# Kernel tuning notes

Measured on AMD Instinct MI355X. Metric: run time of the kernel, lower is better.

Reference implementation:

```python
import jax, jax.numpy as jnp
import numpy as np

D = 384      # embedding_dim (module-level global)
H = 6        # num_heads
HD = D // H  # head_size = 64
T = 256      # block_size (tril buffer cap)
B = 128


def _layernorm(x, gamma, beta, eps=1e-5):
    mu = jnp.mean(x, axis=-1, keepdims=True)
    var = jnp.var(x, axis=-1, keepdims=True)
    return (x - mu) * jax.lax.rsqrt(var + eps) * gamma + beta


def setup_inputs() -> dict:
    key = jax.random.key(0)
    ks = jax.random.split(key, 12)
    s = 0.02
    return {
        "x":   jax.random.normal(ks[0], (B, T, D), jnp.float32),
        "Wq":  jax.random.normal(ks[1], (H, D, HD), jnp.float32) * s,
        "Wk":  jax.random.normal(ks[2], (H, D, HD), jnp.float32) * s,
        "Wv":  jax.random.normal(ks[3], (H, D, HD), jnp.float32) * s,
        "Wp":  jax.random.normal(ks[4], (D, D), jnp.float32) * s,
        "bp":  jnp.zeros((D,), jnp.float32),
        "W1":  jax.random.normal(ks[5], (D, 4 * D), jnp.float32) * s,
        "b1":  jnp.zeros((4 * D,), jnp.float32),
        "W2":  jax.random.normal(ks[6], (4 * D, D), jnp.float32) * s,
        "b2":  jnp.zeros((D,), jnp.float32),
        "g1":  jnp.ones((D,), jnp.float32),
        "be1": jnp.zeros((D,), jnp.float32),
        "g2":  jnp.ones((D,), jnp.float32),
        "be2": jnp.zeros((D,), jnp.float32),
    }


def reference(x, Wq, Wk, Wv, Wp, bp, W1, b1, W2, b2, g1, be1, g2, be2):
    Bsz, Tlen, C = x.shape
    # pre-LN self-attention
    h = _layernorm(x, g1, be1)
    q = jnp.einsum("btd,hdk->bhtk", h, Wq)
    k = jnp.einsum("bsd,hdk->bhsk", h, Wk)
    v = jnp.einsum("bsd,hdk->bhsk", h, Wv)
    # NOTE: source divides by sqrt(C)=sqrt(embedding_dim), not sqrt(head_size)
    scores = jnp.einsum("bhtk,bhsk->bhts", q, k) / jnp.sqrt(jnp.float32(C))
    causal = jnp.tril(jnp.ones((Tlen, Tlen), bool))
    scores = jnp.where(causal, scores, jnp.float32(-jnp.inf))
    attn = jax.nn.softmax(scores, axis=-1)          # dropout = identity (eval)
    o = jnp.einsum("bhts,bhsk->bhtk", attn, v)      # [B,H,T,HD]
    o = o.transpose(0, 2, 1, 3).reshape(Bsz, Tlen, C)  # concat heads
    sa = o @ Wp + bp
    x = x + sa
    # pre-LN feed-forward
    h2 = _layernorm(x, g2, be2)
    ff = jax.nn.relu(h2 @ W1 + b1) @ W2 + b2
    return x + ff
```

## Files before the change

### kernel.cpp

```cpp
#include <hip/hip_runtime.h>
#include <cstdint>
#include <cstddef>

#define D_   384
#define Hn   6
#define HDm  64
#define T_   256
#define B_   128
#define NROW (B_ * T_)

typedef __bf16  bf16x8 __attribute__((ext_vector_type(8)));
typedef float   f32x4  __attribute__((ext_vector_type(4)));
typedef const __attribute__((address_space(1))) void gvoid;
typedef __attribute__((address_space(3))) void lvoid;

__device__ inline uint32_t bf16rn(float f) {
  uint32_t u = __float_as_uint(f);
  return (u + 0x7FFFu + ((u >> 16) & 1u)) >> 16;
}

__global__ __launch_bounds__(128) void ln_kernel(const float* __restrict__ x,
                                                 const float* __restrict__ g,
                                                 const float* __restrict__ b,
                                                 uint16_t* __restrict__ out) {
  int row = blockIdx.x, tid = threadIdx.x;
  const float* xr = x + (size_t)row * D_;
  float v0 = xr[tid], v1 = xr[tid + 128], v2 = xr[tid + 256];
  float s  = v0 + v1 + v2;
  float ss = v0 * v0 + v1 * v1 + v2 * v2;
#pragma unroll
  for (int off = 32; off > 0; off >>= 1) {
    s  += __shfl_down(s, off);
    ss += __shfl_down(ss, off);
  }
  __shared__ float red[4];
  if ((tid & 63) == 0) { red[(tid >> 6) * 2] = s; red[(tid >> 6) * 2 + 1] = ss; }
  __syncthreads();
  float S = red[0] + red[2], SS = red[1] + red[3];
  float mu  = S * (1.0f / D_);
  float var = SS * (1.0f / D_) - mu * mu;
  float inv = rsqrtf(var + 1e-5f);
  uint16_t* orow = out + (size_t)row * D_;
  orow[tid]       = (uint16_t)bf16rn((v0 - mu) * inv * g[tid]       + b[tid]);
  orow[tid + 128] = (uint16_t)bf16rn((v1 - mu) * inv * g[tid + 128] + b[tid + 128]);
  orow[tid + 256] = (uint16_t)bf16rn((v2 - mu) * inv * g[tid + 256] + b[tid + 256]);
}

__global__ __launch_bounds__(256) void pack_qkv_w(const float* __restrict__ Wq,
                                                  const float* __restrict__ Wk,
                                                  const float* __restrict__ Wv,
                                                  uint16_t* __restrict__ Wo) {
  int idx = blockIdx.x * 256 + threadIdx.x;
  if (idx >= 1152 * D_) return;
  int col = idx / D_, d = idx % D_;
  int which = col / 384, c2 = col % 384;
  int h = c2 / HDm, k = c2 % HDm;
  const float* W = (which == 0) ? Wq : (which == 1) ? Wk : Wv;
  Wo[idx] = (uint16_t)bf16rn(W[((size_t)h * D_ + d) * HDm + k]);
}

__global__ __launch_bounds__(256) void pack_wt(const float* __restrict__ W,
                                               uint16_t* __restrict__ Wt,
                                               int K, int N) {
  int idx = blockIdx.x * 256 + threadIdx.x;
  if (idx >= K * N) return;
  int n = idx / K, k = idx % K;
  Wt[idx] = (uint16_t)bf16rn(W[(size_t)k * N + n]);
}

__global__ __launch_bounds__(256) void gemm_bf16(const uint16_t* __restrict__ A,
                                                 const uint16_t* __restrict__ Bt,
                                                 const float* __restrict__ bias,
                                                 const float* __restrict__ resid,
                                                 void* __restrict__ Cout,
                                                 int M, int N, int K,
                                                 int relu, int store_f32) {
  __shared__ uint16_t As[128 * 32];
  __shared__ uint16_t Bs[128 * 32];
  int tid = threadIdx.x;
  int bm = blockIdx.y * 128, bn = blockIdx.x * 128;
  int lane = tid & 63, wave = tid >> 6;
  int wm = (wave >> 1) << 6;
  int wn = (wave & 1) << 6;
  int lr = lane & 15;
  int lk = (lane >> 4) << 3;
  int r0 = (lane >> 4) << 2;

  f32x4 acc[4][4];
  const f32x4 zero = {0.f, 0.f, 0.f, 0.f};
#pragma unroll
  for (int i = 0; i < 4; ++i)
#pragma unroll
    for (int j = 0; j < 4; ++j) acc[i][j] = zero;

  for (int k0 = 0; k0 < K; k0 += 32) {
    __syncthreads();
#pragma unroll
    for (int t = 0; t < 2; ++t) {
      int c = t * 256 + tid;
      int row = c >> 2, kc = (c & 3) << 3;
      const uint16_t* ga = A  + (size_t)(bm + row) * K + (k0 + kc);
      const uint16_t* gb = Bt + (size_t)(bn + row) * K + (k0 + kc);
      __builtin_amdgcn_global_load_lds((gvoid*)ga, (lvoid*)((char*)As + c * 16), 16, 0, 0);
      __builtin_amdgcn_global_load_lds((gvoid*)gb, (lvoid*)((char*)Bs + c * 16), 16, 0, 0);
    }
    __syncthreads();

    bf16x8 af[4], bfr[4];
#pragma unroll
    for (int i = 0; i < 4; ++i)
      af[i] = *(const bf16x8*)&As[(wm + i * 16 + lr) * 32 + lk];
#pragma unroll
    for (int j = 0; j < 4; ++j)
      bfr[j] = *(const bf16x8*)&Bs[(wn + j * 16 + lr) * 32 + lk];
#pragma unroll
    for (int i = 0; i < 4; ++i)
#pragma unroll
      for (int j = 0; j < 4; ++j)
        acc[i][j] = __builtin_amdgcn_mfma_f32_16x16x32_bf16(af[i], bfr[j], acc[i][j], 0, 0, 0);
  }

#pragma unroll
  for (int i = 0; i < 4; ++i) {
#pragma unroll
    for (int r = 0; r < 4; ++r) {
      int rr = bm + wm + i * 16 + r0 + r;
#pragma unroll
      for (int j = 0; j < 4; ++j) {
        int col = bn + wn + j * 16 + lr;
        float v = acc[i][j][r];
        if (bias)  v += bias[col];
        if (relu)  v = fmaxf(v, 0.0f);
        if (resid) v += resid[(size_t)rr * N + col];
        if (store_f32) ((float*)Cout)[(size_t)rr * N + col] = v;
        else           ((uint16_t*)Cout)[(size_t)rr * N + col] = (uint16_t)bf16rn(v);
      }
    }
  }
}

__global__ __launch_bounds__(256, 2) void attn_mfma(const uint16_t* __restrict__ qkv,
                                                    uint16_t* __restrict__ o) {
  __shared__ uint16_t Kt[64 * 72];
  __shared__ uint16_t Vt[64 * 72];
  __shared__ uint16_t Pb[4 * 64 * 72];
  int bh = blockIdx.x;
  int b = bh / Hn, h = bh % Hn;
  int tid = threadIdx.x;
  int lane = tid & 63, w = tid >> 6;
  int ln = lane & 15, q = lane >> 4;
  int kq = q * 8;
  int m0 = w * 64;
  const uint16_t* base = qkv + (size_t)b * T_ * 1152;

  bf16x8 af[4][2];
#pragma unroll
  for (int i = 0; i < 4; ++i)
#pragma unroll
    for (int ks = 0; ks < 2; ++ks)
      af[i][ks] = *(const bf16x8*)(base + (size_t)(m0 + i * 16 + ln) * 1152 + h * HDm + ks * 32 + kq);

  f32x4 o_[4][4], m_[4], l_[4];
  const f32x4 zero = {0.f, 0.f, 0.f, 0.f};
#pragma unroll
  for (int i = 0; i < 4; ++i) {
    m_[i] = {-1e30f, -1e30f, -1e30f, -1e30f};
    l_[i] = zero;
#pragma unroll
    for (int n = 0; n < 4; ++n) o_[i][n] = zero;
  }
  const float cs = 0.07362222f;

  for (int jt = 0; jt < 4; ++jt) {
    if (jt) __syncthreads();
#pragma unroll
    for (int t = 0; t < 2; ++t) {
      int c = t * 256 + tid;
      int s = c >> 3, d0 = (c & 7) << 3;
      *(uint4*)&Kt[s * 72 + d0] =
          *(const uint4*)(base + (size_t)(jt * 64 + s) * 1152 + 384 + h * HDm + d0);
    }
    {
      int sv = tid & 63, dv = (tid >> 6) << 4;
      const uint16_t* gv = base + (size_t)(jt * 64 + sv) * 1152 + 768 + h * HDm + dv;
      uint16_t tmp[16];
      *(uint4*)&tmp[0] = *(const uint4*)gv;
      *(uint4*)&tmp[8] = *(const uint4*)(gv + 8);
#pragma unroll
      for (int jj = 0; jj < 16; ++jj) Vt[(dv + jj) * 72 + sv] = tmp[jj];
    }
    __syncthreads();

    if (w >= jt) {
      f32x4 s2[4][4];
#pragma unroll
      for (int i = 0; i < 4; ++i)
#pragma unroll
        for (int j = 0; j < 4; ++j) s2[i][j] = zero;
#pragma unroll
      for (int ks = 0; ks < 2; ++ks) {
        bf16x8 bf[4];
#pragma unroll
        for (int j = 0; j < 4; ++j)
          bf[j] = *(const bf16x8*)&Kt[(j * 16 + ln) * 72 + ks * 32 + kq];
#pragma unroll
        for (int i = 0; i < 4; ++i)
#pragma unroll
          for (int j = 0; j < 4; ++j)
            s2[i][j] = __builtin_amdgcn_mfma_f32_16x16x32_bf16(af[i][ks], bf[j], s2[i][j], 0, 0, 0);
      }
#pragma unroll
      for (int i = 0; i < 4; ++i) {
#pragma unroll
        for (int j = 0; j < 4; ++j)
#pragma unroll
          for (int r = 0; r < 4; ++r) s2[i][j][r] *= cs;
        if (jt == w) {
#pragma unroll
          for (int j = 0; j < 4; ++j)
#pragma unroll
            for (int r = 0; r < 4; ++r)
              if (j * 16 + ln > i * 16 + q * 4 + r) s2[i][j][r] = -1e30f;
        }
        f32x4 rm;
#pragma unroll
        for (int r = 0; r < 4; ++r)
          rm[r] = fmaxf(fmaxf(s2[i][0][r], s2[i][1][r]), fmaxf(s2[i][2][r], s2[i][3][r]));
#pragma unroll
        for (int off = 1; off < 16; off <<= 1)
#pragma unroll
          for (int r = 0; r < 4; ++r)
            rm[r] = fmaxf(rm[r], __shfl_xor(rm[r], off));
        f32x4 mn, al, ps;
#pragma unroll
        for (int r = 0; r < 4; ++r) {
          mn[r] = fmaxf(m_[i][r], rm[r]);
          al[r] = exp2f(m_[i][r] - mn[r]);
          ps[r] = 0.f;
        }
        m_[i] = mn;
#pragma unroll
        for (int j = 0; j < 4; ++j)
#pragma unroll
          for (int r = 0; r < 4; ++r) {
            float p = exp2f(s2[i][j][r] - mn[r]);
            s2[i][j][r] = p;
            ps[r] += p;
          }
#pragma unroll
        for (int r = 0; r < 4; ++r) l_[i][r] = l_[i][r] * al[r] + ps[r];
#pragma unroll
        for (int n = 0; n < 4; ++n)
#pragma unroll
          for (int r = 0; r < 4; ++r) o_[i][n][r] *= al[r];
#pragma unroll
        for (int j = 0; j < 4; ++j)
#pragma unroll
          for (int r = 0; r < 4; ++r)
            Pb[w * 4608 + (i * 16 + q * 4 + r) * 72 + j * 16 + ln] =
                (uint16_t)bf16rn(s2[i][j][r]);
      }
      bf16x8 pa[4][2];
#pragma unroll
      for (int i = 0; i < 4; ++i)
#pragma unroll
        for (int ks = 0; ks < 2; ++ks)
          pa[i][ks] = *(const bf16x8*)&Pb[w * 4608 + (i * 16 + ln) * 72 + ks * 32 + kq];
#pragma unroll
      for (int n = 0; n < 4; ++n) {
        bf16x8 bv0 = *(const bf16x8*)&Vt[(n * 16 + ln) * 72 + kq];
        bf16x8 bv1 = *(const bf16x8*)&Vt[(n * 16 + ln) * 72 + 32 + kq];
#pragma unroll
        for (int i = 0; i < 4; ++i) {
          o_[i][n] = __builtin_amdgcn_mfma_f32_16x16x32_bf16(pa[i][0], bv0, o_[i][n], 0, 0, 0);
          o_[i][n] = __builtin_amdgcn_mfma_f32_16x16x32_bf16(pa[i][1], bv1, o_[i][n], 0, 0, 0);
        }
      }
    }
  }
#pragma unroll
  for (int i = 0; i < 4; ++i) {
    f32x4 lt = l_[i];
#pragma unroll
    for (int off = 1; off < 16; off <<= 1)
#pragma unroll
      for (int r = 0; r < 4; ++r) lt[r] += __shfl_xor(lt[r], off);
#pragma unroll
    for (int r = 0; r < 4; ++r) {
      float inv = 1.0f / lt[r];
      int row = b * T_ + m0 + i * 16 + q * 4 + r;
      uint16_t* op = o + (size_t)row * D_ + h * HDm;
#pragma unroll
      for (int n = 0; n < 4; ++n)
        op[n * 16 + ln] = (uint16_t)bf16rn(o_[i][n][r] * inv);
    }
  }
}

extern "C" void kernel_launch(void* const* d_in, const int* in_sizes, int n_in,
                              void* d_out, int out_size, void* d_ws, size_t ws_size,
                              hipStream_t stream) {
  const float* x   = (const float*)d_in[0];
  const float* Wq  = (const float*)d_in[1];
  const float* Wk  = (const float*)d_in[2];
  const float* Wv  = (const float*)d_in[3];
  const float* Wp  = (const float*)d_in[4];
  const float* bp  = (const float*)d_in[5];
  const float* W1  = (const float*)d_in[6];
  const float* b1  = (const float*)d_in[7];
  const float* W2  = (const float*)d_in[8];
  const float* b2  = (const float*)d_in[9];
  const float* g1  = (const float*)d_in[10];
  const float* be1 = (const float*)d_in[11];
  const float* g2  = (const float*)d_in[12];
  const float* be2 = (const float*)d_in[13];
  float* out = (float*)d_out;

  char* ws = (char*)d_ws;
  uint16_t* hbuf  = (uint16_t*)ws;
  uint16_t* qkv   = (uint16_t*)(ws + 25165824ull);
  uint16_t* ob    = (uint16_t*)(ws + 100663296ull);
  uint16_t* ff1   = qkv;
  uint16_t* Wqkvt = (uint16_t*)(ws + 125829120ull);
  uint16_t* Wpt   = (uint16_t*)(ws + 126713856ull);
  uint16_t* W1t   = (uint16_t*)(ws + 127008768ull);
  uint16_t* W2t   = (uint16_t*)(ws + 128188416ull);

  pack_qkv_w<<<(1152 * D_ + 255) / 256, 256, 0, stream>>>(Wq, Wk, Wv, Wqkvt);
  pack_wt<<<(384 * 384 + 255) / 256, 256, 0, stream>>>(Wp, Wpt, 384, 384);
  pack_wt<<<(384 * 1536 + 255) / 256, 256, 0, stream>>>(W1, W1t, 384, 1536);
  pack_wt<<<(1536 * 384 + 255) / 256, 256, 0, stream>>>(W2, W2t, 1536, 384);
  ln_kernel<<<NROW, 128, 0, stream>>>(x, g1, be1, hbuf);
  gemm_bf16<<<dim3(1152 / 128, NROW / 128), 256, 0, stream>>>(
      hbuf, Wqkvt, nullptr, nullptr, qkv, NROW, 1152, 384, 0, 0);
  attn_mfma<<<B_ * Hn, 256, 0, stream>>>(qkv, ob);
  gemm_bf16<<<dim3(384 / 128, NROW / 128), 256, 0, stream>>>(
      ob, Wpt, bp, x, out, NROW, 384, 384, 0, 1);
  ln_kernel<<<NROW, 128, 0, stream>>>(out, g2, be2, hbuf);
  gemm_bf16<<<dim3(1536 / 128, NROW / 128), 256, 0, stream>>>(
      hbuf, W1t, b1, nullptr, ff1, NROW, 1536, 384, 1, 0);
  gemm_bf16<<<dim3(384 / 128, NROW / 128), 256, 0, stream>>>(
      ff1, W2t, b2, out, out, NROW, 384, 1536, 0, 1);
}
```

Measured before the change: 550.5 us.

## Deepen GEMM K-tile to 64 with XOR-swizzled LDS and swap grid axes

The bf16 GEMM now stages 64-wide K slices per iteration instead of 32. Each 16-byte chunk is stored in LDS at an XOR-swizzled column position (chunk ^ row&7), so fragment reads avoid bank conflicts. This halves the number of barrier/load phases per K and doubles the MFMAs between syncs. The grid is also transposed so consecutive blocks walk along M with the same N tile, which changes which tiles are resident in L2 together. LDS use doubles to 32KB per block, which may lower occupancy.

```diff
diff --git a/kernel.cpp b/kernel.cpp
--- a/kernel.cpp
+++ b/kernel.cpp
@@ -75,16 +75,17 @@
                                                  void* __restrict__ Cout,
                                                  int M, int N, int K,
                                                  int relu, int store_f32) {
-  __shared__ uint16_t As[128 * 32];
-  __shared__ uint16_t Bs[128 * 32];
+  __shared__ uint16_t As[128 * 64];
+  __shared__ uint16_t Bs[128 * 64];
   int tid = threadIdx.x;
-  int bm = blockIdx.y * 128, bn = blockIdx.x * 128;
+  int bm = blockIdx.x * 128, bn = blockIdx.y * 128;
   int lane = tid & 63, wave = tid >> 6;
   int wm = (wave >> 1) << 6;
   int wn = (wave & 1) << 6;
   int lr = lane & 15;
-  int lk = (lane >> 4) << 3;
-  int r0 = (lane >> 4) << 2;
+  int q  = lane >> 4;
+  int r0 = q << 2;
+  int sw = lr & 7;
 
   f32x4 acc[4][4];
   const f32x4 zero = {0.f, 0.f, 0.f, 0.f};
@@ -93,31 +94,40 @@
 #pragma unroll
     for (int j = 0; j < 4; ++j) acc[i][j] = zero;
 
-  for (int k0 = 0; k0 < K; k0 += 32) {
+  int c0a = (q ^ sw) << 3;
+  int c1a = ((4 | q) ^ sw) << 3;
+
+  for (int k0 = 0; k0 < K; k0 += 64) {
     __syncthreads();
 #pragma unroll
-    for (int t = 0; t < 2; ++t) {
+    for (int t = 0; t < 4; ++t) {
       int c = t * 256 + tid;
-      int row = c >> 2, kc = (c & 3) << 3;
-      const uint16_t* ga = A  + (size_t)(bm + row) * K + (k0 + kc);
-      const uint16_t* gb = Bt + (size_t)(bn + row) * K + (k0 + kc);
+      int row = c >> 3, cc = c & 7;
+      int gc = cc ^ (row & 7);
+      const uint16_t* ga = A  + (size_t)(bm + row) * K + (k0 + gc * 8);
+      const uint16_t* gb = Bt + (size_t)(bn + row) * K + (k0 + gc * 8);
       __builtin_amdgcn_global_load_lds((gvoid*)ga, (lvoid*)((char*)As + c * 16), 16, 0, 0);
       __builtin_amdgcn_global_load_lds((gvoid*)gb, (lvoid*)((char*)Bs + c * 16), 16, 0, 0);
     }
     __syncthreads();
 
-    bf16x8 af[4], bfr[4];
-#pragma unroll
-    for (int i = 0; i < 4; ++i)
-      af[i] = *(const bf16x8*)&As[(wm + i * 16 + lr) * 32 + lk];
-#pragma unroll
-    for (int j = 0; j < 4; ++j)
-      bfr[j] = *(const bf16x8*)&Bs[(wn + j * 16 + lr) * 32 + lk];
-#pragma unroll
-    for (int i = 0; i < 4; ++i)
-#pragma unroll
-      for (int j = 0; j < 4; ++j)
-        acc[i][j] = __builtin_amdgcn_mfma_f32_16x16x32_bf16(af[i], bfr[j], acc[i][j], 0, 0, 0);
+    bf16x8 af[2][4], bfr[2][4];
+#pragma unroll
+    for (int i = 0; i < 4; ++i) {
+      int ra = (wm + i * 16 + lr) * 64;
+      af[0][i] = *(const bf16x8*)&As[ra + c0a];
+      af[1][i] = *(const bf16x8*)&As[ra + c1a];
+      int rb = (wn + i * 16 + lr) * 64;
+      bfr[0][i] = *(const bf16x8*)&Bs[rb + c0a];
+      bfr[1][i] = *(const bf16x8*)&Bs[rb + c1a];
+    }
+#pragma unroll
+    for (int ks = 0; ks < 2; ++ks)
+#pragma unroll
+      for (int i = 0; i < 4; ++i)
+#pragma unroll
+        for (int j = 0; j < 4; ++j)
+          acc[i][j] = __builtin_amdgcn_mfma_f32_16x16x32_bf16(af[ks][i], bfr[ks][j], acc[i][j], 0, 0, 0);
   }
 
 #pragma unroll
@@ -331,14 +341,14 @@
   pack_wt<<<(384 * 1536 + 255) / 256, 256, 0, stream>>>(W1, W1t, 384, 1536);
   pack_wt<<<(1536 * 384 + 255) / 256, 256, 0, stream>>>(W2, W2t, 1536, 384);
   ln_kernel<<<NROW, 128, 0, stream>>>(x, g1, be1, hbuf);
-  gemm_bf16<<<dim3(1152 / 128, NROW / 128), 256, 0, stream>>>(
+  gemm_bf16<<<dim3(NROW / 128, 1152 / 128), 256, 0, stream>>>(
       hbuf, Wqkvt, nullptr, nullptr, qkv, NROW, 1152, 384, 0, 0);
   attn_mfma<<<B_ * Hn, 256, 0, stream>>>(qkv, ob);
-  gemm_bf16<<<dim3(384 / 128, NROW / 128), 256, 0, stream>>>(
+  gemm_bf16<<<dim3(NROW / 128, 384 / 128), 256, 0, stream>>>(
       ob, Wpt, bp, x, out, NROW, 384, 384, 0, 1);
   ln_kernel<<<NROW, 128, 0, stream>>>(out, g2, be2, hbuf);
-  gemm_bf16<<<dim3(1536 / 128, NROW / 128), 256, 0, stream>>>(
+  gemm_bf16<<<dim3(NROW / 128, 1536 / 128), 256, 0, stream>>>(
       hbuf, W1t, b1, nullptr, ff1, NROW, 1536, 384, 1, 0);
-  gemm_bf16<<<dim3(384 / 128, NROW / 128), 256, 0, stream>>>(
+  gemm_bf16<<<dim3(NROW / 128, 384 / 128), 256, 0, stream>>>(
       ff1, W2t, b2, out, out, NROW, 384, 1536, 0, 1);
 }
```

Result: slower. 638.9 us (+16.1%).
